# Kernel tuning notes

Measured on AMD Instinct MI355X. Metric: run time of the kernel, lower is better.

## Reference

```python
import jax, jax.numpy as jnp
import numpy as np

N, B, F, E, C, H = 2048, 64, 48, 65536, 7, 20


def _gcn_norm(row, col, n):
    # gcn_norm(add_self_loops=False): deg over target (col), norm = d^-1/2[row]*d^-1/2[col]
    deg = jnp.zeros((n,), jnp.float32).at[col].add(1.0)
    dinv = jnp.where(deg > 0, 1.0 / jnp.sqrt(jnp.maximum(deg, 1e-12)), 0.0)
    return dinv[row] * dinv[col]


def _arma(x, W, V, b, row, col, norm, act):
    # ARMAConv, num_stacks=1, num_layers=1, shared_weights, dropout inactive (eval):
    # out = act( A_hat @ (x W) + x V + b )
    h = jnp.einsum('bnf,fo->bno', x, W)                     # [B,N,O]
    msg = h[:, row, :] * norm[None, :, None]                # gather along nodes
    agg = jnp.zeros_like(h).at[:, col, :].add(msg)          # scatter-add to targets
    return act(agg + jnp.einsum('bnf,fo->bno', x, V) + b)


_gelu = lambda z: jax.nn.gelu(z, approximate=False)
_relu = jax.nn.relu
# nn.Softmax() with dim=None on a 3-D tensor -> legacy dim=0
_sm0 = lambda z: jax.nn.softmax(z, axis=0)


def setup_inputs() -> dict:
    key = jax.random.key(0)
    ks = jax.random.split(key, 30)
    feat = lambda k: jax.random.normal(k, (N, B, F), jnp.float32)
    edges = lambda k: jax.random.randint(k, (2, E), 0, N, jnp.int64)
    s = 0.05
    return {
        'A_input': edges(ks[0]), 'A_week_input': edges(ks[1]),
        'A_weekend_input': edges(ks[2]), 'Location_location_input': edges(ks[3]),
        'Temporal_input': feat(ks[4]), 'Temporal_week_input': feat(ks[5]),
        'Temporal_weekend_input': feat(ks[6]), 'Distance_input': feat(ks[7]),
        'Duration_input': feat(ks[8]), 'Location_time_input': feat(ks[9]),
        # 6 first-layer ARMAConvs (F->H), branch order:
        # 0 temporal, 1 week, 2 weekend, 3 distance, 4 duration, 5 location_location
        'W1': jax.random.normal(ks[10], (6, F, H), jnp.float32) * s,
        'V1': jax.random.normal(ks[11], (6, F, H), jnp.float32) * s,
        'b1': jax.random.normal(ks[12], (6, H), jnp.float32) * s,
        # 6 in-forward ARMAConvs (H->C)
        'W2': jax.random.normal(ks[13], (6, H, C), jnp.float32) * s,
        'V2': jax.random.normal(ks[14], (6, H, C), jnp.float32) * s,
        'b2': jax.random.normal(ks[15], (6, C), jnp.float32) * s,
        'Wlt': jax.random.normal(ks[16], (F, 40), jnp.float32) * s,
        'blt': jax.random.normal(ks[17], (40,), jnp.float32) * s,
        'Wl2': jax.random.normal(ks[18], (40, C), jnp.float32) * s,
        'bl2': jax.random.normal(ks[19], (C,), jnp.float32) * s,
        'Wd': jax.random.normal(ks[20], (C, C), jnp.float32) * s,
        'bd': jax.random.normal(ks[21], (C,), jnp.float32) * s,
        'Wg': jax.random.normal(ks[22], (C, C), jnp.float32) * s,
        'bg': jax.random.normal(ks[23], (C,), jnp.float32) * s,
    }


def _branch(x, i, row, col, norm, W1, V1, b1, W2, V2, b2):
    y = jax.nn.elu(_arma(x, W1[i], V1[i], b1[i], row, col, norm, _gelu))
    return _sm0(_arma(y, W2[i], V2[i], b2[i], row, col, norm, _relu))


def reference(A_input, A_week_input, A_weekend_input, Location_location_input,
              Temporal_input, Temporal_week_input, Temporal_weekend_input,
              Distance_input, Duration_input, Location_time_input,
              W1, V1, b1, W2, V2, b2, Wlt, blt, Wl2, bl2, Wd, bd, Wg, bg):
    perm = lambda t: jnp.transpose(t, (1, 0, 2))  # [N,B,F] -> [B,N,F]
    rA, cA = A_input[0], A_input[1]
    rW, cW = A_week_input[0], A_week_input[1]
    rE, cE = A_weekend_input[0], A_weekend_input[1]
    rL, cL = Location_location_input[0], Location_location_input[1]
    nA, nW, nE, nL = (_gcn_norm(rA, cA, N), _gcn_norm(rW, cW, N),
                      _gcn_norm(rE, cE, N), _gcn_norm(rL, cL, N))
    p = (W1, V1, b1, W2, V2, b2)
    o_t = _branch(perm(Temporal_input), 0, rA, cA, nA, *p)
    o_w = _branch(perm(Temporal_week_input), 1, rW, cW, nW, *p)
    o_e = _branch(perm(Temporal_weekend_input), 2, rE, cE, nE, *p)
    o_d = _branch(perm(Distance_input), 3, rA, cA, nA, *p)
    o_u = _branch(perm(Duration_input), 4, rA, cA, nA, *p)
    xlt = perm(Location_time_input)
    o_l = _branch(xlt, 5, rL, cL, nL, *p)
    o_lt = _sm0((xlt @ Wlt + blt) @ Wl2 + bl2)
    out_dense = _sm0((2.0 * o_l + 2.0 * o_lt) @ Wd + bd)
    out_gnn = _sm0((o_t + o_w + o_e + o_d + o_u) @ Wg + bg)
    return jnp.transpose(out_dense + out_gnn, (1, 2, 0))  # [B,N,C] -> [N,C,B]
```

## Files before the change

### kernel.cpp

```cpp
#include <hip/hip_runtime.h>
#include <math.h>

#define NN   2048
#define BB   64
#define FF   48
#define EE   65536
#define CC   7
#define HH   20

#define OFF_DEG      0u
#define OFF_CURSOR   32768u
#define ZBYTES       65536u
#define OFF_DINV     65536u
#define OFF_ROWPTR   98304u
#define OFF_CSRC     131584u
#define OFF_CSRW     1180160u
#define OFF_H1       2228736u
#define OFF_P        OFF_H1
#define OFF_Y        65143296u
#define OFF_H2       128057856u
#define OFF_YV       153223680u
#define OFF_T        175243776u

#define H1S  2621440u
#define H2S  1048576u
#define YVS  917504u

typedef __attribute__((ext_vector_type(8))) short bf16x8;
typedef __attribute__((ext_vector_type(4))) float f32x4;
#define MFMA32 __builtin_amdgcn_mfma_f32_16x16x32_bf16

__device__ __forceinline__ unsigned short bf16_rne(float x) {
    unsigned u = __float_as_uint(x);
    u += 0x7fffu + ((u >> 16) & 1u);
    return (unsigned short)(u >> 16);
}
__device__ __forceinline__ float4 ubf4(uint2 u) {
    float4 r;
    r.x = __uint_as_float(u.x << 16);
    r.y = __uint_as_float(u.x & 0xffff0000u);
    r.z = __uint_as_float(u.y << 16);
    r.w = __uint_as_float(u.y & 0xffff0000u);
    return r;
}

__global__ __launch_bounds__(256) void count_deg_kernel(
    const int* __restrict__ c0, const int* __restrict__ c1,
    const int* __restrict__ c2, const int* __restrict__ c3, int* __restrict__ deg)
{
    int idx = blockIdx.x * 256 + threadIdx.x;
    int g = idx >> 16, e = idx & 0xFFFF;
    const int* cp = g == 0 ? c0 : g == 1 ? c1 : g == 2 ? c2 : c3;
    atomicAdd(&deg[(g << 11) + cp[e]], 1);
}

__global__ __launch_bounds__(256) void scan_dinv_kernel(
    const int* __restrict__ deg, int* __restrict__ rowptr, float* __restrict__ dinv)
{
    int g = blockIdx.x, t = threadIdx.x;
    __shared__ int part[256];
    const int* d = deg + g * NN;
    int loc[8]; int s = 0;
#pragma unroll
    for (int j = 0; j < 8; ++j) { loc[j] = d[t * 8 + j]; s += loc[j]; }
    part[t] = s; __syncthreads();
    for (int off = 1; off < 256; off <<= 1) {
        int v = (t >= off) ? part[t - off] : 0;
        __syncthreads();
        part[t] += v;
        __syncthreads();
    }
    int run = (t > 0) ? part[t - 1] : 0;
    int* rp = rowptr + g * (NN + 1);
#pragma unroll
    for (int j = 0; j < 8; ++j) {
        int n = t * 8 + j;
        rp[n] = run; run += loc[j];
        dinv[g * NN + n] = loc[j] > 0 ? 1.0f / sqrtf((float)loc[j]) : 0.0f;
    }
    if (t == 255) rp[NN] = run;
}

__global__ __launch_bounds__(256) void fill_csr_kernel(
    const int* __restrict__ r0, const int* __restrict__ c0,
    const int* __restrict__ r1, const int* __restrict__ c1,
    const int* __restrict__ r2, const int* __restrict__ c2,
    const int* __restrict__ r3, const int* __restrict__ c3,
    const int* __restrict__ rowptr, int* __restrict__ cursor,
    const float* __restrict__ dinv, int* __restrict__ csrc, float* __restrict__ cw)
{
    int idx = blockIdx.x * 256 + threadIdx.x;
    int g = idx >> 16, e = idx & 0xFFFF;
    const int* rp = g == 0 ? r0 : g == 1 ? r1 : g == 2 ? r2 : r3;
    const int* cp = g == 0 ? c0 : g == 1 ? c1 : g == 2 ? c2 : c3;
    int r = rp[e], c = cp[e];
    int pos = atomicAdd(&cursor[(g << 11) + c], 1);
    int o = rowptr[g * (NN + 1) + c] + pos;
    csrc[(g << 16) + o] = r;
    cw[(g << 16) + o] = dinv[(g << 11) + r] * dinv[(g << 11) + c];
}

__global__ __launch_bounds__(256) void gemm48_mfma(
    const float* __restrict__ X0, const float* __restrict__ X1,
    const float* __restrict__ X2, const float* __restrict__ X3,
    const float* __restrict__ X4, const float* __restrict__ X5,
    const float* __restrict__ W1, const float* __restrict__ V1,
    const float* __restrict__ b1,
    unsigned short* __restrict__ H1u, unsigned short* __restrict__ Yu)
{
    int br = blockIdx.y;
    const float* X = br == 0 ? X0 : br == 1 ? X1 : br == 2 ? X2 :
                     br == 3 ? X3 : br == 4 ? X4 : X5;
    const float* Wa = W1 + br * 960;
    const float* Wb = V1 + br * 960;

    int t = threadIdx.x;
    int w = t >> 6, lane = t & 63;
    int node = blockIdx.x * 4 + w;
    int col = lane & 15;
    int grp = lane >> 4;

    bf16x8 bw[2][2], bv[2][2];
#pragma unroll
    for (int c = 0; c < 2; ++c)
#pragma unroll
        for (int nt = 0; nt < 2; ++nt) {
            int n = nt * 16 + col;
#pragma unroll
            for (int j = 0; j < 8; ++j) {
                int k = c * 32 + grp * 8 + j;
                float vw = 0.0f, vv = 0.0f;
                if (n < 20 && k < 48) { vw = Wa[k * 20 + n]; vv = Wb[k * 20 + n]; }
                bw[c][nt][j] = (short)bf16_rne(vw);
                bv[c][nt][j] = (short)bf16_rne(vv);
            }
        }
    float bias0 = b1[br * 20 + col];
    float bias1 = col < 4 ? b1[br * 20 + 16 + col] : 0.0f;

#pragma unroll
    for (int tb = 0; tb < 4; ++tb) {
        int b0 = tb * 16;
        const float* xr = X + ((size_t)node * 64 + b0 + col) * 48;

        bf16x8 a0;
        {
            float4 xa = *reinterpret_cast<const float4*>(xr + grp * 8);
            float4 xb = *reinterpret_cast<const float4*>(xr + grp * 8 + 4);
            a0[0] = (short)bf16_rne(xa.x); a0[1] = (short)bf16_rne(xa.y);
            a0[2] = (short)bf16_rne(xa.z); a0[3] = (short)bf16_rne(xa.w);
            a0[4] = (short)bf16_rne(xb.x); a0[5] = (short)bf16_rne(xb.y);
            a0[6] = (short)bf16_rne(xb.z); a0[7] = (short)bf16_rne(xb.w);
        }
        bf16x8 a1 = {0, 0, 0, 0, 0, 0, 0, 0};
        if (grp < 2) {
            float4 xc = *reinterpret_cast<const float4*>(xr + 32 + grp * 8);
            float4 xd = *reinterpret_cast<const float4*>(xr + 32 + grp * 8 + 4);
            a1[0] = (short)bf16_rne(xc.x); a1[1] = (short)bf16_rne(xc.y);
            a1[2] = (short)bf16_rne(xc.z); a1[3] = (short)bf16_rne(xc.w);
            a1[4] = (short)bf16_rne(xd.x); a1[5] = (short)bf16_rne(xd.y);
            a1[6] = (short)bf16_rne(xd.z); a1[7] = (short)bf16_rne(xd.w);
        }

        f32x4 aw0 = {0,0,0,0}, aw1 = {0,0,0,0}, av0 = {0,0,0,0}, av1 = {0,0,0,0};
        aw0 = MFMA32(a0, bw[0][0], aw0, 0, 0, 0);
        aw1 = MFMA32(a0, bw[0][1], aw1, 0, 0, 0);
        av0 = MFMA32(a0, bv[0][0], av0, 0, 0, 0);
        av1 = MFMA32(a0, bv[0][1], av1, 0, 0, 0);
        aw0 = MFMA32(a1, bw[1][0], aw0, 0, 0, 0);
        aw1 = MFMA32(a1, bw[1][1], aw1, 0, 0, 0);
        av0 = MFMA32(a1, bv[1][0], av0, 0, 0, 0);
        av1 = MFMA32(a1, bv[1][1], av1, 0, 0, 0);

        size_t base = (size_t)br * H1S + (size_t)node * 1280 + b0 + grp * 4;
        uint2 pk;
        pk.x = (unsigned)bf16_rne(aw0[0]) | ((unsigned)bf16_rne(aw0[1]) << 16);
        pk.y = (unsigned)bf16_rne(aw0[2]) | ((unsigned)bf16_rne(aw0[3]) << 16);
        *reinterpret_cast<uint2*>(H1u + base + (size_t)col * 64) = pk;
        pk.x = (unsigned)bf16_rne(av0[0] + bias0) | ((unsigned)bf16_rne(av0[1] + bias0) << 16);
        pk.y = (unsigned)bf16_rne(av0[2] + bias0) | ((unsigned)bf16_rne(av0[3] + bias0) << 16);
        *reinterpret_cast<uint2*>(Yu + base + (size_t)col * 64) = pk;
        if (col < 4) {
            int k2 = 16 + col;
            pk.x = (unsigned)bf16_rne(aw1[0]) | ((unsigned)bf16_rne(aw1[1]) << 16);
            pk.y = (unsigned)bf16_rne(aw1[2]) | ((unsigned)bf16_rne(aw1[3]) << 16);
            *reinterpret_cast<uint2*>(H1u + base + (size_t)k2 * 64) = pk;
            pk.x = (unsigned)bf16_rne(av1[0] + bias1) | ((unsigned)bf16_rne(av1[1] + bias1) << 16);
            pk.y = (unsigned)bf16_rne(av1[2] + bias1) | ((unsigned)bf16_rne(av1[3] + bias1) << 16);
            *reinterpret_cast<uint2*>(Yu + base + (size_t)k2 * 64) = pk;
        }
    }
}

__global__ __launch_bounds__(512, 4) void gemm48_lt(
    const float* __restrict__ X, const float* __restrict__ Wlt,
    const float* __restrict__ blt, float* __restrict__ T)
{
    __shared__ float xs[512 * 24];
    int t = threadIdx.x;
    const float4* Xv = reinterpret_cast<const float4*>(X) + (size_t)blockIdx.x * 6144;

    int r = t & 255;
    int kb = __builtin_amdgcn_readfirstlane((t >> 8) * 10);
    const float* wap = Wlt + kb;
    const float* wbp = Wlt + 20 + kb;

    float accA[2][10], accB[2][10];
#pragma unroll
    for (int j = 0; j < 10; ++j) {
        accA[0][j] = blt[kb + j];      accA[1][j] = accA[0][j];
        accB[0][j] = blt[20 + kb + j]; accB[1][j] = accB[0][j];
    }

#pragma unroll
    for (int ph = 0; ph < 2; ++ph) {
        if (ph) __syncthreads();
#pragma unroll
        for (int i = 0; i < 6; ++i) {
            int fl4 = i * 512 + t;
            int rr = fl4 / 6, fq = fl4 - rr * 6;
            float4 v = Xv[rr * 12 + ph * 6 + fq];
            *reinterpret_cast<float4*>(&xs[fl4 * 4]) = v;
        }
        __syncthreads();
#pragma unroll
        for (int fq = 0; fq < 6; ++fq) {
            float4 xA = *reinterpret_cast<const float4*>(&xs[r * 24 + fq * 4]);
            float4 xB = *reinterpret_cast<const float4*>(&xs[(r + 256) * 24 + fq * 4]);
#pragma unroll
            for (int ff = 0; ff < 4; ++ff) {
                int f = ph * 24 + fq * 4 + ff;
                float a0 = ff == 0 ? xA.x : ff == 1 ? xA.y : ff == 2 ? xA.z : xA.w;
                float a1 = ff == 0 ? xB.x : ff == 1 ? xB.y : ff == 2 ? xB.z : xB.w;
                const float* wr = wap + f * 40;
                const float* vr = wbp + f * 40;
#pragma unroll
                for (int j = 0; j < 10; ++j) {
                    float w = wr[j], v2 = vr[j];
                    accA[0][j] += w * a0;  accA[1][j] += w * a1;
                    accB[0][j] += v2 * a0; accB[1][j] += v2 * a1;
                }
            }
        }
    }

    int n0 = blockIdx.x * 8;
#pragma unroll
    for (int rr = 0; rr < 2; ++rr) {
        int row = r + rr * 256;
        int n = n0 + (row >> 6), b = row & 63;
        size_t base = (size_t)n * 2560 + b;
#pragma unroll
        for (int j = 0; j < 10; ++j) {
            T[base + (size_t)(kb + j) * 64] = accA[rr][j];
            T[base + (size_t)(20 + kb + j) * 64] = accB[rr][j];
        }
    }
}

__device__ __forceinline__ void fma4(float4& a, float w, const float4 v) {
    a.x += w * v.x; a.y += w * v.y; a.z += w * v.z; a.w += w * v.w;
}
__device__ __forceinline__ float gelu_elu(float v) {
    float g = 0.5f * v * (1.0f + erff(v * 0.70710678118654752f));
    return g > 0.0f ? g : expm1f(g);
}

__global__ __launch_bounds__(256) void spmm1_all(
    const uint2* __restrict__ H1u, uint2* __restrict__ Y,
    const int* __restrict__ rowptr, const int* __restrict__ csrc, const float* __restrict__ csrw)
{
    int bid = blockIdx.x;
    int w0 = (bid & 7) * 1920 + (bid >> 3);
    int sl = w0 >> 9;
    int ng = w0 & 511;
    int br = sl / 5, q = sl - br * 5;

    int gg = br == 1 ? 1 : br == 2 ? 2 : br == 5 ? 3 : 0;
    const int*   rp  = rowptr + gg * (NN + 1);
    const int*   src = csrc + (size_t)gg * EE;
    const float* wts = csrw + (size_t)gg * EE;
    const uint2* h = H1u + (size_t)br * (H1S / 4);
    uint2*       y = Y + (size_t)br * (H1S / 4);

    int wv = __builtin_amdgcn_readfirstlane(threadIdx.x >> 6);
    int lane = threadIdx.x & 63;
    int n = ng * 4 + wv;
    int off = q * 64 + lane;
    int s0 = rp[n], s1 = rp[n + 1];

    float4 a0 = {0,0,0,0}, a1 = {0,0,0,0}, a2 = {0,0,0,0}, a3 = {0,0,0,0};
    int e = s0;
    for (; e + 8 <= s1; e += 8) {
        int   iA = src[e],   iB = src[e+1], iC = src[e+2], iD = src[e+3];
        int   iE = src[e+4], iF = src[e+5], iG = src[e+6], iH = src[e+7];
        float wA = wts[e],   wB = wts[e+1], wC = wts[e+2], wD = wts[e+3];
        float wE = wts[e+4], wF = wts[e+5], wG = wts[e+6], wH = wts[e+7];
        uint2 u0 = h[iA * 320 + off];
        uint2 u1 = h[iB * 320 + off];
        uint2 u2 = h[iC * 320 + off];
        uint2 u3 = h[iD * 320 + off];
        uint2 u4 = h[iE * 320 + off];
        uint2 u5 = h[iF * 320 + off];
        uint2 u6 = h[iG * 320 + off];
        uint2 u7 = h[iH * 320 + off];
        fma4(a0, wA, ubf4(u0)); fma4(a1, wB, ubf4(u1));
        fma4(a2, wC, ubf4(u2)); fma4(a3, wD, ubf4(u3));
        fma4(a0, wE, ubf4(u4)); fma4(a1, wF, ubf4(u5));
        fma4(a2, wG, ubf4(u6)); fma4(a3, wH, ubf4(u7));
    }
    for (; e + 2 <= s1; e += 2) {
        uint2 u0 = h[src[e] * 320 + off];
        uint2 u1 = h[src[e+1] * 320 + off];
        fma4(a0, wts[e], ubf4(u0)); fma4(a1, wts[e+1], ubf4(u1));
    }
    if (e < s1) fma4(a0, wts[e], ubf4(h[src[e] * 320 + off]));
    a0.x += a1.x + a2.x + a3.x;
    a0.y += a1.y + a2.y + a3.y;
    a0.z += a1.z + a2.z + a3.z;
    a0.w += a1.w + a2.w + a3.w;

    size_t b0 = (size_t)n * 320 + off;
    float4 xv = ubf4(y[b0]);
    float4 r;
    r.x = gelu_elu(a0.x + xv.x);
    r.y = gelu_elu(a0.y + xv.y);
    r.z = gelu_elu(a0.z + xv.z);
    r.w = gelu_elu(a0.w + xv.w);
    uint2 pk;
    pk.x = (unsigned)bf16_rne(r.x) | ((unsigned)bf16_rne(r.y) << 16);
    pk.y = (unsigned)bf16_rne(r.z) | ((unsigned)bf16_rne(r.w) << 16);
    y[b0] = pk;
}

__global__ __launch_bounds__(256) void gemm2_all(
    const unsigned short* __restrict__ Yu, const float* __restrict__ W2,
    const float* __restrict__ V2, const float* __restrict__ b2,
    unsigned short* __restrict__ H2u, float* __restrict__ YV)
{
    int br = blockIdx.y;
    const unsigned short* y = Yu + (size_t)br * H1S;
    unsigned short* h2 = H2u + (size_t)br * H2S;
    float* yv = YV + (size_t)br * YVS;
    __shared__ float w2s[140], v2s[140], b2s[7];
    int t = threadIdx.x;
    if (t < 140) { w2s[t] = W2[br * 140 + t]; v2s[t] = V2[br * 140 + t]; }
    if (t < 7) b2s[t] = b2[br * 7 + t];
    __syncthreads();
    int wv = __builtin_amdgcn_readfirstlane(t >> 6), b = t & 63;
    int n = blockIdx.x * 4 + wv;
    size_t yb = (size_t)n * 1280 + b;
    float yr[20];
#pragma unroll
    for (int k = 0; k < 20; ++k)
        yr[k] = __uint_as_float((unsigned)y[yb + (size_t)k * 64] << 16);
    float a[7] = {}, v[7] = {};
#pragma unroll
    for (int k = 0; k < 20; ++k) {
        float yk = yr[k];
#pragma unroll
        for (int c = 0; c < 7; ++c) {
            a[c] += yk * w2s[k * 7 + c];
            v[c] += yk * v2s[k * 7 + c];
        }
    }
    size_t hb = (size_t)n * 512 + b;
#pragma unroll
    for (int c = 0; c < 7; ++c) h2[hb + (size_t)c * 64] = bf16_rne(a[c]);
    h2[hb + 7 * 64] = 0;
    size_t vb = (size_t)n * 448 + b;
#pragma unroll
    for (int c = 0; c < 7; ++c) yv[vb + (size_t)c * 64] = v[c] + b2s[c];
}

__global__ __launch_bounds__(256) void spmm2_all(
    const uint2* __restrict__ H2u, const float* __restrict__ YV,
    const int* __restrict__ rowptr, const int* __restrict__ csrc, const float* __restrict__ csrw,
    float* __restrict__ P)
{
    int bid = blockIdx.x;
    int w0 = (bid & 7) * 768 + (bid >> 3);
    int sl = w0 >> 9;
    int ng = w0 & 511;
    int br = sl >> 1, hh = sl & 1;

    int gg = br == 1 ? 1 : br == 2 ? 2 : br == 5 ? 3 : 0;
    const int*   rp  = rowptr + gg * (NN + 1);
    const int*   src = csrc + (size_t)gg * EE;
    const float* wts = csrw + (size_t)gg * EE;
    const uint2* h2 = H2u + (size_t)br * (H2S / 4);
    const float* yv = YV + (size_t)br * YVS;
    float* p = P + (size_t)br * YVS;

    int wv = __builtin_amdgcn_readfirstlane(threadIdx.x >> 6);
    int lane = threadIdx.x & 63;
    int n = ng * 4 + wv;
    int s = hh * 64 + lane;
    int c = s >> 4;
    int bq = lane & 15;
    int s0 = rp[n], s1 = rp[n + 1];

    float4 a0 = {0,0,0,0}, a1 = {0,0,0,0}, a2 = {0,0,0,0}, a3 = {0,0,0,0};
    int e = s0;
    for (; e + 8 <= s1; e += 8) {
        int   iA = src[e],   iB = src[e+1], iC = src[e+2], iD = src[e+3];
        int   iE = src[e+4], iF = src[e+5], iG = src[e+6], iH = src[e+7];
        float wA = wts[e],   wB = wts[e+1], wC = wts[e+2], wD = wts[e+3];
        float wE = wts[e+4], wF = wts[e+5], wG = wts[e+6], wH = wts[e+7];
        uint2 u0 = h2[iA * 128 + s];
        uint2 u1 = h2[iB * 128 + s];
        uint2 u2 = h2[iC * 128 + s];
        uint2 u3 = h2[iD * 128 + s];
        uint2 u4 = h2[iE * 128 + s];
        uint2 u5 = h2[iF * 128 + s];
        uint2 u6 = h2[iG * 128 + s];
        uint2 u7 = h2[iH * 128 + s];
        fma4(a0, wA, ubf4(u0)); fma4(a1, wB, ubf4(u1));
        fma4(a2, wC, ubf4(u2)); fma4(a3, wD, ubf4(u3));
        fma4(a0, wE, ubf4(u4)); fma4(a1, wF, ubf4(u5));
        fma4(a2, wG, ubf4(u6)); fma4(a3, wH, ubf4(u7));
    }
    for (; e < s1; ++e) fma4(a0, wts[e], ubf4(h2[src[e] * 128 + s]));
    a0.x += a1.x + a2.x + a3.x;
    a0.y += a1.y + a2.y + a3.y;
    a0.z += a1.z + a2.z + a3.z;
    a0.w += a1.w + a2.w + a3.w;

    float4 z = {0,0,0,0};
    if (c < 7) {
        float4 yvv = *reinterpret_cast<const float4*>(&yv[(size_t)n * 448 + c * 64 + bq * 4]);
        z.x = fmaxf(a0.x + yvv.x, 0.0f);
        z.y = fmaxf(a0.y + yvv.y, 0.0f);
        z.z = fmaxf(a0.z + yvv.z, 0.0f);
        z.w = fmaxf(a0.w + yvv.w, 0.0f);
    }
    float m = fmaxf(fmaxf(z.x, z.y), fmaxf(z.z, z.w));
#pragma unroll
    for (int o = 8; o > 0; o >>= 1) m = fmaxf(m, __shfl_xor(m, o, 64));
    float4 pz;
    pz.x = expf(z.x - m); pz.y = expf(z.y - m);
    pz.z = expf(z.z - m); pz.w = expf(z.w - m);
    float sm = pz.x + pz.y + pz.z + pz.w;
#pragma unroll
    for (int o = 8; o > 0; o >>= 1) sm += __shfl_xor(sm, o, 64);
    float inv = 1.0f / sm;
    if (c < 7) {
        float4 r = { pz.x * inv, pz.y * inv, pz.z * inv, pz.w * inv };
        *reinterpret_cast<float4*>(&p[(size_t)n * 448 + c * 64 + bq * 4]) = r;
    }
}

__device__ __forceinline__ void wave_softmax7(float* z)
{
#pragma unroll
    for (int c = 0; c < 7; ++c) {
        float m = z[c];
#pragma unroll
        for (int o = 32; o > 0; o >>= 1) m = fmaxf(m, __shfl_xor(m, o, 64));
        float p = expf(z[c] - m);
        float s = p;
#pragma unroll
        for (int o = 32; o > 0; o >>= 1) s += __shfl_xor(s, o, 64);
        z[c] = p / s;
    }
}

__global__ __launch_bounds__(256) void combine_kernel(
    const float* __restrict__ T, const float* __restrict__ P,
    const float* __restrict__ Wl2, const float* __restrict__ bl2,
    const float* __restrict__ Wd, const float* __restrict__ bd,
    const float* __restrict__ Wg, const float* __restrict__ bg,
    float* __restrict__ out)
{
    __shared__ float wl2s[280], bl2s[7], wds[49], bds[7], wgs[49], bgs[7];
    int t = threadIdx.x;
    for (int i = t; i < 280; i += 256) wl2s[i] = Wl2[i];
    if (t < 49) { wds[t] = Wd[t]; wgs[t] = Wg[t]; }
    if (t < 7) { bl2s[t] = bl2[t]; bds[t] = bd[t]; bgs[t] = bg[t]; }
    __syncthreads();

    int wv = t >> 6, b = t & 63;
    int n = blockIdx.x * 4 + wv;
    size_t rbase = (size_t)n * 2560 + b;
    float tr[40];
#pragma unroll
    for (int j = 0; j < 40; ++j) tr[j] = T[rbase + (size_t)j * 64];

    float u[7];
#pragma unroll
    for (int c = 0; c < 7; ++c) u[c] = bl2s[c];
    for (int j = 0; j < 40; ++j) {
        float tv = tr[j];
#pragma unroll
        for (int c = 0; c < 7; ++c) u[c] += tv * wl2s[j * 7 + c];
    }
    wave_softmax7(u);

    size_t sbase = (size_t)n * 448 + b;
    float sd[7], sg[7];
#pragma unroll
    for (int c = 0; c < 7; ++c) {
        size_t o = sbase + (size_t)c * 64;
        sg[c] = P[o] + P[YVS + o] + P[2 * YVS + o] + P[3 * YVS + o] + P[4 * YVS + o];
        sd[c] = 2.0f * P[5 * YVS + o] + 2.0f * u[c];
    }
    float dv[7];
#pragma unroll
    for (int c = 0; c < 7; ++c) dv[c] = bds[c];
#pragma unroll
    for (int c2 = 0; c2 < 7; ++c2) {
        float s = sd[c2];
#pragma unroll
        for (int c = 0; c < 7; ++c) dv[c] += s * wds[c2 * 7 + c];
    }
    wave_softmax7(dv);

    float gv[7];
#pragma unroll
    for (int c = 0; c < 7; ++c) gv[c] = bgs[c];
#pragma unroll
    for (int c2 = 0; c2 < 7; ++c2) {
        float s = sg[c2];
#pragma unroll
        for (int c = 0; c < 7; ++c) gv[c] += s * wgs[c2 * 7 + c];
    }
    wave_softmax7(gv);

    size_t ob = (size_t)n * 448 + b;
#pragma unroll
    for (int c = 0; c < 7; ++c) out[ob + (size_t)c * 64] = dv[c] + gv[c];
}

extern "C" void kernel_launch(void* const* d_in, const int* in_sizes, int n_in,
                              void* d_out, int out_size, void* d_ws, size_t ws_size,
                              hipStream_t stream)
{
    (void)in_sizes; (void)n_in; (void)out_size; (void)ws_size;
    const int* e0 = (const int*)d_in[0];
    const int* e1 = (const int*)d_in[1];
    const int* e2 = (const int*)d_in[2];
    const int* e3 = (const int*)d_in[3];
    const float* X0 = (const float*)d_in[4];
    const float* X1 = (const float*)d_in[5];
    const float* X2 = (const float*)d_in[6];
    const float* X3 = (const float*)d_in[7];
    const float* X4 = (const float*)d_in[8];
    const float* X5 = (const float*)d_in[9];
    const float* W1  = (const float*)d_in[10];
    const float* V1  = (const float*)d_in[11];
    const float* b1  = (const float*)d_in[12];
    const float* W2  = (const float*)d_in[13];
    const float* V2  = (const float*)d_in[14];
    const float* b2  = (const float*)d_in[15];
    const float* Wlt = (const float*)d_in[16];
    const float* blt = (const float*)d_in[17];
    const float* Wl2 = (const float*)d_in[18];
    const float* bl2 = (const float*)d_in[19];
    const float* Wd  = (const float*)d_in[20];
    const float* bd  = (const float*)d_in[21];
    const float* Wg  = (const float*)d_in[22];
    const float* bg  = (const float*)d_in[23];

    char* ws = (char*)d_ws;
    int*   deg    = (int*)(ws + OFF_DEG);
    int*   cursor = (int*)(ws + OFF_CURSOR);
    float* dinv   = (float*)(ws + OFF_DINV);
    int*   rowptr = (int*)(ws + OFF_ROWPTR);
    int*   csrc   = (int*)(ws + OFF_CSRC);
    float* csrw   = (float*)(ws + OFF_CSRW);
    unsigned short* H1u = (unsigned short*)(ws + OFF_H1);
    float* Pbuf   = (float*)(ws + OFF_P);
    unsigned short* Yu = (unsigned short*)(ws + OFF_Y);
    unsigned short* H2u = (unsigned short*)(ws + OFF_H2);
    float* YV     = (float*)(ws + OFF_YV);
    float* Tbuf   = (float*)(ws + OFF_T);

    hipMemsetAsync(d_ws, 0, ZBYTES, stream);

    count_deg_kernel<<<1024, 256, 0, stream>>>(e0 + EE, e1 + EE, e2 + EE, e3 + EE, deg);
    scan_dinv_kernel<<<4, 256, 0, stream>>>(deg, rowptr, dinv);
    fill_csr_kernel<<<1024, 256, 0, stream>>>(e0, e0 + EE, e1, e1 + EE, e2, e2 + EE,
                                              e3, e3 + EE, rowptr, cursor, dinv, csrc, csrw);

    gemm48_mfma<<<dim3(512, 6), 256, 0, stream>>>(X0, X1, X2, X3, X4, X5,
                                                  W1, V1, b1, H1u, Yu);
    gemm48_lt<<<256, 512, 0, stream>>>(X5, Wlt, blt, Tbuf);
    spmm1_all<<<15360, 256, 0, stream>>>((const uint2*)H1u, (uint2*)Yu,
                                         rowptr, csrc, csrw);
    gemm2_all<<<dim3(512, 6), 256, 0, stream>>>(Yu, W2, V2, b2, H2u, YV);
    spmm2_all<<<6144, 256, 0, stream>>>((const uint2*)H2u, YV,
                                        rowptr, csrc, csrw, Pbuf);
    combine_kernel<<<512, 256, 0, stream>>>(Tbuf, Pbuf, Wl2, bl2, Wd, bd, Wg, bg,
                                            (float*)d_out);
}
```

Baseline: 254.6 us.

## Fuse location-time projection into the MFMA first-layer GEMM via extra grid slice

Merges the separate FP32 gemm48_lt kernel into gemm48_mfma as a seventh blockIdx.y slice that computes X5·Wlt+blt with bf16 MFMA. X tiles are now staged through padded shared memory with coalesced float4 loads instead of strided per-lane global reads. This removes one launch and lets the two GEMMs share a single wave of blocks. The cost is bf16 rounding on the lt path (previously fp32), an extra shared-memory footprint per block, and X5 being read twice.

```diff
diff --git a/kernel.cpp b/kernel.cpp
--- a/kernel.cpp
+++ b/kernel.cpp
@@ -106,154 +106,171 @@
     const float* __restrict__ X4, const float* __restrict__ X5,
     const float* __restrict__ W1, const float* __restrict__ V1,
     const float* __restrict__ b1,
-    unsigned short* __restrict__ H1u, unsigned short* __restrict__ Yu)
+    const float* __restrict__ Wlt, const float* __restrict__ blt,
+    unsigned short* __restrict__ H1u, unsigned short* __restrict__ Yu,
+    float* __restrict__ T)
 {
     int br = blockIdx.y;
     const float* X = br == 0 ? X0 : br == 1 ? X1 : br == 2 ? X2 :
                      br == 3 ? X3 : br == 4 ? X4 : X5;
-    const float* Wa = W1 + br * 960;
-    const float* Wb = V1 + br * 960;
-
+
+    __shared__ float xs[256 * 52];
     int t = threadIdx.x;
+    const float4* Xv = reinterpret_cast<const float4*>(X) + (size_t)blockIdx.x * 3072;
+
+#pragma unroll
+    for (int i = 0; i < 12; ++i) {
+        int fl4 = i * 256 + t;
+        float4 v = Xv[fl4];
+        int r = fl4 / 12, fq = fl4 % 12;
+        *reinterpret_cast<float4*>(&xs[r * 52 + fq * 4]) = v;
+    }
+
     int w = t >> 6, lane = t & 63;
     int node = blockIdx.x * 4 + w;
     int col = lane & 15;
     int grp = lane >> 4;
 
-    bf16x8 bw[2][2], bv[2][2];
-#pragma unroll
-    for (int c = 0; c < 2; ++c)
-#pragma unroll
-        for (int nt = 0; nt < 2; ++nt) {
+    if (br < 6) {
+        const float* Wa = W1 + br * 960;
+        const float* Wb = V1 + br * 960;
+        bf16x8 bw[2][2], bv[2][2];
+#pragma unroll
+        for (int c = 0; c < 2; ++c)
+#pragma unroll
+            for (int nt = 0; nt < 2; ++nt) {
+                int n = nt * 16 + col;
+#pragma unroll
+                for (int j = 0; j < 8; ++j) {
+                    int k = c * 32 + grp * 8 + j;
+                    float vw = 0.0f, vv = 0.0f;
+                    if (n < 20 && k < 48) { vw = Wa[k * 20 + n]; vv = Wb[k * 20 + n]; }
+                    bw[c][nt][j] = (short)bf16_rne(vw);
+                    bv[c][nt][j] = (short)bf16_rne(vv);
+                }
+            }
+        float bias0 = b1[br * 20 + col];
+        float bias1 = col < 4 ? b1[br * 20 + 16 + col] : 0.0f;
+        __syncthreads();
+
+#pragma unroll
+        for (int tb = 0; tb < 4; ++tb) {
+            int b0 = tb * 16;
+            int row = w * 64 + b0 + col;
+            const float* xr = &xs[row * 52];
+
+            bf16x8 a0;
+            {
+                float4 xa = *reinterpret_cast<const float4*>(xr + grp * 8);
+                float4 xb = *reinterpret_cast<const float4*>(xr + grp * 8 + 4);
+                a0[0] = (short)bf16_rne(xa.x); a0[1] = (short)bf16_rne(xa.y);
+                a0[2] = (short)bf16_rne(xa.z); a0[3] = (short)bf16_rne(xa.w);
+                a0[4] = (short)bf16_rne(xb.x); a0[5] = (short)bf16_rne(xb.y);
+                a0[6] = (short)bf16_rne(xb.z); a0[7] = (short)bf16_rne(xb.w);
+            }
+            bf16x8 a1 = {0, 0, 0, 0, 0, 0, 0, 0};
+            if (grp < 2) {
+                float4 xc = *reinterpret_cast<const float4*>(xr + 32 + grp * 8);
+                float4 xd = *reinterpret_cast<const float4*>(xr + 32 + grp * 8 + 4);
+                a1[0] = (short)bf16_rne(xc.x); a1[1] = (short)bf16_rne(xc.y);
+                a1[2] = (short)bf16_rne(xc.z); a1[3] = (short)bf16_rne(xc.w);
+                a1[4] = (short)bf16_rne(xd.x); a1[5] = (short)bf16_rne(xd.y);
+                a1[6] = (short)bf16_rne(xd.z); a1[7] = (short)bf16_rne(xd.w);
+            }
+
+            f32x4 aw0 = {0,0,0,0}, aw1 = {0,0,0,0}, av0 = {0,0,0,0}, av1 = {0,0,0,0};
+            aw0 = MFMA32(a0, bw[0][0], aw0, 0, 0, 0);
+            aw1 = MFMA32(a0, bw[0][1], aw1, 0, 0, 0);
+            av0 = MFMA32(a0, bv[0][0], av0, 0, 0, 0);
+            av1 = MFMA32(a0, bv[0][1], av1, 0, 0, 0);
+            aw0 = MFMA32(a1, bw[1][0], aw0, 0, 0, 0);
+            aw1 = MFMA32(a1, bw[1][1], aw1, 0, 0, 0);
+            av0 = MFMA32(a1, bv[1][0], av0, 0, 0, 0);
+            av1 = MFMA32(a1, bv[1][1], av1, 0, 0, 0);
+
+            size_t base = (size_t)br * H1S + (size_t)node * 1280 + b0 + grp * 4;
+            uint2 pk;
+            pk.x = (unsigned)bf16_rne(aw0[0]) | ((unsigned)bf16_rne(aw0[1]) << 16);
+            pk.y = (unsigned)bf16_rne(aw0[2]) | ((unsigned)bf16_rne(aw0[3]) << 16);
+            *reinterpret_cast<uint2*>(H1u + base + (size_t)col * 64) = pk;
+            pk.x = (unsigned)bf16_rne(av0[0] + bias0) | ((unsigned)bf16_rne(av0[1] + bias0) << 16);
+            pk.y = (unsigned)bf16_rne(av0[2] + bias0) | ((unsigned)bf16_rne(av0[3] + bias0) << 16);
+            *reinterpret_cast<uint2*>(Yu + base + (size_t)col * 64) = pk;
+            if (col < 4) {
+                int k2 = 16 + col;
+                pk.x = (unsigned)bf16_rne(aw1[0]) | ((unsigned)bf16_rne(aw1[1]) << 16);
+                pk.y = (unsigned)bf16_rne(aw1[2]) | ((unsigned)bf16_rne(aw1[3]) << 16);
+                *reinterpret_cast<uint2*>(H1u + base + (size_t)k2 * 64) = pk;
+                pk.x = (unsigned)bf16_rne(av1[0] + bias1) | ((unsigned)bf16_rne(av1[1] + bias1) << 16);
+                pk.y = (unsigned)bf16_rne(av1[2] + bias1) | ((unsigned)bf16_rne(av1[3] + bias1) << 16);
+                *reinterpret_cast<uint2*>(Yu + base + (size_t)k2 * 64) = pk;
+            }
+        }
+    } else {
+        bf16x8 bw[2][3];
+#pragma unroll
+        for (int c = 0; c < 2; ++c)
+#pragma unroll
+            for (int nt = 0; nt < 3; ++nt) {
+                int n = nt * 16 + col;
+#pragma unroll
+                for (int j = 0; j < 8; ++j) {
+                    int k = c * 32 + grp * 8 + j;
+                    float vw = 0.0f;
+                    if (n < 40 && k < 48) vw = Wlt[k * 40 + n];
+                    bw[c][nt][j] = (short)bf16_rne(vw);
+                }
+            }
+        float bias[3];
+#pragma unroll
+        for (int nt = 0; nt < 3; ++nt) {
             int n = nt * 16 + col;
-#pragma unroll
-            for (int j = 0; j < 8; ++j) {
-                int k = c * 32 + grp * 8 + j;
-                float vw = 0.0f, vv = 0.0f;
-                if (n < 20 && k < 48) { vw = Wa[k * 20 + n]; vv = Wb[k * 20 + n]; }
-                bw[c][nt][j] = (short)bf16_rne(vw);
-                bv[c][nt][j] = (short)bf16_rne(vv);
-            }
-        }
-    float bias0 = b1[br * 20 + col];
-    float bias1 = col < 4 ? b1[br * 20 + 16 + col] : 0.0f;
-
-#pragma unroll
-    for (int tb = 0; tb < 4; ++tb) {
-        int b0 = tb * 16;
-        const float* xr = X + ((size_t)node * 64 + b0 + col) * 48;
-
-        bf16x8 a0;
-        {
-            float4 xa = *reinterpret_cast<const float4*>(xr + grp * 8);
-            float4 xb = *reinterpret_cast<const float4*>(xr + grp * 8 + 4);
-            a0[0] = (short)bf16_rne(xa.x); a0[1] = (short)bf16_rne(xa.y);
-            a0[2] = (short)bf16_rne(xa.z); a0[3] = (short)bf16_rne(xa.w);
-            a0[4] = (short)bf16_rne(xb.x); a0[5] = (short)bf16_rne(xb.y);
-            a0[6] = (short)bf16_rne(xb.z); a0[7] = (short)bf16_rne(xb.w);
-        }
-        bf16x8 a1 = {0, 0, 0, 0, 0, 0, 0, 0};
-        if (grp < 2) {
-            float4 xc = *reinterpret_cast<const float4*>(xr + 32 + grp * 8);
-            float4 xd = *reinterpret_cast<const float4*>(xr + 32 + grp * 8 + 4);
-            a1[0] = (short)bf16_rne(xc.x); a1[1] = (short)bf16_rne(xc.y);
-            a1[2] = (short)bf16_rne(xc.z); a1[3] = (short)bf16_rne(xc.w);
-            a1[4] = (short)bf16_rne(xd.x); a1[5] = (short)bf16_rne(xd.y);
-            a1[6] = (short)bf16_rne(xd.z); a1[7] = (short)bf16_rne(xd.w);
-        }
-
-        f32x4 aw0 = {0,0,0,0}, aw1 = {0,0,0,0}, av0 = {0,0,0,0}, av1 = {0,0,0,0};
-        aw0 = MFMA32(a0, bw[0][0], aw0, 0, 0, 0);
-        aw1 = MFMA32(a0, bw[0][1], aw1, 0, 0, 0);
-        av0 = MFMA32(a0, bv[0][0], av0, 0, 0, 0);
-        av1 = MFMA32(a0, bv[0][1], av1, 0, 0, 0);
-        aw0 = MFMA32(a1, bw[1][0], aw0, 0, 0, 0);
-        aw1 = MFMA32(a1, bw[1][1], aw1, 0, 0, 0);
-        av0 = MFMA32(a1, bv[1][0], av0, 0, 0, 0);
-        av1 = MFMA32(a1, bv[1][1], av1, 0, 0, 0);
-
-        size_t base = (size_t)br * H1S + (size_t)node * 1280 + b0 + grp * 4;
-        uint2 pk;
-        pk.x = (unsigned)bf16_rne(aw0[0]) | ((unsigned)bf16_rne(aw0[1]) << 16);
-        pk.y = (unsigned)bf16_rne(aw0[2]) | ((unsigned)bf16_rne(aw0[3]) << 16);
-        *reinterpret_cast<uint2*>(H1u + base + (size_t)col * 64) = pk;
-        pk.x = (unsigned)bf16_rne(av0[0] + bias0) | ((unsigned)bf16_rne(av0[1] + bias0) << 16);
-        pk.y = (unsigned)bf16_rne(av0[2] + bias0) | ((unsigned)bf16_rne(av0[3] + bias0) << 16);
-        *reinterpret_cast<uint2*>(Yu + base + (size_t)col * 64) = pk;
-        if (col < 4) {
-            int k2 = 16 + col;
-            pk.x = (unsigned)bf16_rne(aw1[0]) | ((unsigned)bf16_rne(aw1[1]) << 16);
-            pk.y = (unsigned)bf16_rne(aw1[2]) | ((unsigned)bf16_rne(aw1[3]) << 16);
-            *reinterpret_cast<uint2*>(H1u + base + (size_t)k2 * 64) = pk;
-            pk.x = (unsigned)bf16_rne(av1[0] + bias1) | ((unsigned)bf16_rne(av1[1] + bias1) << 16);
-            pk.y = (unsigned)bf16_rne(av1[2] + bias1) | ((unsigned)bf16_rne(av1[3] + bias1) << 16);
-            *reinterpret_cast<uint2*>(Yu + base + (size_t)k2 * 64) = pk;
-        }
-    }
-}
-
-__global__ __launch_bounds__(512, 4) void gemm48_lt(
-    const float* __restrict__ X, const float* __restrict__ Wlt,
-    const float* __restrict__ blt, float* __restrict__ T)
-{
-    __shared__ float xs[512 * 24];
-    int t = threadIdx.x;
-    const float4* Xv = reinterpret_cast<const float4*>(X) + (size_t)blockIdx.x * 6144;
-
-    int r = t & 255;
-    int kb = __builtin_amdgcn_readfirstlane((t >> 8) * 10);
-    const float* wap = Wlt + kb;
-    const float* wbp = Wlt + 20 + kb;
-
-    float accA[2][10], accB[2][10];
-#pragma unroll
-    for (int j = 0; j < 10; ++j) {
-        accA[0][j] = blt[kb + j];      accA[1][j] = accA[0][j];
-        accB[0][j] = blt[20 + kb + j]; accB[1][j] = accB[0][j];
-    }
-
-#pragma unroll
-    for (int ph = 0; ph < 2; ++ph) {
-        if (ph) __syncthreads();
-#pragma unroll
-        for (int i = 0; i < 6; ++i) {
-            int fl4 = i * 512 + t;
-            int rr = fl4 / 6, fq = fl4 - rr * 6;
-            float4 v = Xv[rr * 12 + ph * 6 + fq];
-            *reinterpret_cast<float4*>(&xs[fl4 * 4]) = v;
+            bias[nt] = n < 40 ? blt[n] : 0.0f;
         }
         __syncthreads();
-#pragma unroll
-        for (int fq = 0; fq < 6; ++fq) {
-            float4 xA = *reinterpret_cast<const float4*>(&xs[r * 24 + fq * 4]);
-            float4 xB = *reinterpret_cast<const float4*>(&xs[(r + 256) * 24 + fq * 4]);
-#pragma unroll
-            for (int ff = 0; ff < 4; ++ff) {
-                int f = ph * 24 + fq * 4 + ff;
-                float a0 = ff == 0 ? xA.x : ff == 1 ? xA.y : ff == 2 ? xA.z : xA.w;
-                float a1 = ff == 0 ? xB.x : ff == 1 ? xB.y : ff == 2 ? xB.z : xB.w;
-                const float* wr = wap + f * 40;
-                const float* vr = wbp + f * 40;
-#pragma unroll
-                for (int j = 0; j < 10; ++j) {
-                    float w = wr[j], v2 = vr[j];
-                    accA[0][j] += w * a0;  accA[1][j] += w * a1;
-                    accB[0][j] += v2 * a0; accB[1][j] += v2 * a1;
+
+#pragma unroll
+        for (int tb = 0; tb < 4; ++tb) {
+            int b0 = tb * 16;
+            int row = w * 64 + b0 + col;
+            const float* xr = &xs[row * 52];
+
+            bf16x8 a0;
+            {
+                float4 xa = *reinterpret_cast<const float4*>(xr + grp * 8);
+                float4 xb = *reinterpret_cast<const float4*>(xr + grp * 8 + 4);
+                a0[0] = (short)bf16_rne(xa.x); a0[1] = (short)bf16_rne(xa.y);
+                a0[2] = (short)bf16_rne(xa.z); a0[3] = (short)bf16_rne(xa.w);
+                a0[4] = (short)bf16_rne(xb.x); a0[5] = (short)bf16_rne(xb.y);
+                a0[6] = (short)bf16_rne(xb.z); a0[7] = (short)bf16_rne(xb.w);
+            }
+            bf16x8 a1 = {0, 0, 0, 0, 0, 0, 0, 0};
+            if (grp < 2) {
+                float4 xc = *reinterpret_cast<const float4*>(xr + 32 + grp * 8);
+                float4 xd = *reinterpret_cast<const float4*>(xr + 32 + grp * 8 + 4);
+                a1[0] = (short)bf16_rne(xc.x); a1[1] = (short)bf16_rne(xc.y);
+                a1[2] = (short)bf16_rne(xc.z); a1[3] = (short)bf16_rne(xc.w);
+                a1[4] = (short)bf16_rne(xd.x); a1[5] = (short)bf16_rne(xd.y);
+                a1[6] = (short)bf16_rne(xd.z); a1[7] = (short)bf16_rne(xd.w);
+            }
+
+            f32x4 ac[3] = {{0,0,0,0},{0,0,0,0},{0,0,0,0}};
+#pragma unroll
+            for (int nt = 0; nt < 3; ++nt) {
+                ac[nt] = MFMA32(a0, bw[0][nt], ac[nt], 0, 0, 0);
+                ac[nt] = MFMA32(a1, bw[1][nt], ac[nt], 0, 0, 0);
+            }
+
+            size_t base = (size_t)node * 2560 + b0 + grp * 4;
+#pragma unroll
+            for (int nt = 0; nt < 3; ++nt) {
+                int n = nt * 16 + col;
+                if (n < 40) {
+                    float4 v = { ac[nt][0] + bias[nt], ac[nt][1] + bias[nt],
+                                 ac[nt][2] + bias[nt], ac[nt][3] + bias[nt] };
+                    *reinterpret_cast<float4*>(&T[base + (size_t)n * 64]) = v;
                 }
             }
-        }
-    }
-
-    int n0 = blockIdx.x * 8;
-#pragma unroll
-    for (int rr = 0; rr < 2; ++rr) {
-        int row = r + rr * 256;
-        int n = n0 + (row >> 6), b = row & 63;
-        size_t base = (size_t)n * 2560 + b;
-#pragma unroll
-        for (int j = 0; j < 10; ++j) {
-            T[base + (size_t)(kb + j) * 64] = accA[rr][j];
-            T[base + (size_t)(20 + kb + j) * 64] = accB[rr][j];
         }
     }
 }
@@ -582,9 +599,8 @@
     fill_csr_kernel<<<1024, 256, 0, stream>>>(e0, e0 + EE, e1, e1 + EE, e2, e2 + EE,
                                               e3, e3 + EE, rowptr, cursor, dinv, csrc, csrw);
 
-    gemm48_mfma<<<dim3(512, 6), 256, 0, stream>>>(X0, X1, X2, X3, X4, X5,
-                                                  W1, V1, b1, H1u, Yu);
-    gemm48_lt<<<256, 512, 0, stream>>>(X5, Wlt, blt, Tbuf);
+    gemm48_mfma<<<dim3(512, 7), 256, 0, stream>>>(X0, X1, X2, X3, X4, X5,
+                                                  W1, V1, b1, Wlt, blt, H1u, Yu, Tbuf);
     spmm1_all<<<15360, 256, 0, stream>>>((const uint2*)H1u, (uint2*)Yu,
                                          rowptr, csrc, csrw);
     gemm2_all<<<dim3(512, 6), 256, 0, stream>>>(Yu, W2, V2, b2, H2u, YV);
```

Result: faster. 226.1 us (-11.2%).
